# Kernel optimization log

Measured on AMD Instinct MI355X. Metric: run time of the kernel, lower is better.

The kernel has to match this reference:

```python
import jax, jax.numpy as jnp
import numpy as np

N = 50000
E = 500000
H = 128


def _linear(x, w, b):
    # torch nn.Linear: y = x @ W.T + b, W is [out, in]
    return x @ w.T + b


def _layer(x, h, edge_index, w0_w, w0_b, wl_w, wl_b, w1_w, w1_b):
    # PyG MessagePassing(aggr='add', flow='target_to_source'):
    # x_j = h[edge_index[1]], scatter-add into edge_index[0], dim_size = N
    msg = h[edge_index[1]]                               # [E, H] gather
    aggr = jax.ops.segment_sum(msg, edge_index[0], num_segments=h.shape[0])  # [N, H]
    return _linear(aggr, wl_w, wl_b) + _linear(h, w0_w, w0_b) + _linear(x, w1_w, w1_b)


def setup_inputs() -> dict:
    key = jax.random.key(0)
    ks = jax.random.split(key, 12)
    wscale = 0.05
    return {
        "x_a": jax.random.normal(ks[0], (N, H), jnp.float32),
        "x_b": jax.random.normal(ks[1], (N, H), jnp.float32),
        "edge_ab": jax.random.randint(ks[2], (2, E), 0, N, jnp.int32),
        "edge_ba": jax.random.randint(ks[3], (2, E), 0, N, jnp.int32),
        "conv0_w0_w": jax.random.normal(ks[4], (H, H), jnp.float32) * wscale,
        "conv0_w0_b": jnp.zeros((H,), jnp.float32),
        "conv0_wl_w": jax.random.normal(ks[5], (H, H), jnp.float32) * wscale,
        "conv0_wl_b": jnp.zeros((H,), jnp.float32),
        "conv0_w1_w": jax.random.normal(ks[6], (H, H), jnp.float32) * wscale,
        "conv0_w1_b": jnp.zeros((H,), jnp.float32),
        "conv1_w0_w": jax.random.normal(ks[7], (H, H), jnp.float32) * wscale,
        "conv1_w0_b": jnp.zeros((H,), jnp.float32),
        "conv1_wl_w": jax.random.normal(ks[8], (H, H), jnp.float32) * wscale,
        "conv1_wl_b": jnp.zeros((H,), jnp.float32),
        "conv1_w1_w": jax.random.normal(ks[9], (H, H), jnp.float32) * wscale,
        "conv1_w1_b": jnp.zeros((H,), jnp.float32),
        "out_w": jax.random.normal(ks[10], (H, H), jnp.float32) * wscale,
        "out_b": jnp.zeros((H,), jnp.float32),
    }


def reference(x_a, x_b, edge_ab, edge_ba,
              conv0_w0_w, conv0_w0_b, conv0_wl_w, conv0_wl_b, conv0_w1_w, conv0_w1_b,
              conv1_w0_w, conv1_w0_b, conv1_wl_w, conv1_wl_b, conv1_w1_w, conv1_w1_b,
              out_w, out_b):
    # metapath = [(a, r1, b), (b, r2, a)], loop over reversed(metapath):
    # iter 0: conv_idx=1, edge (b, r2, a), dst='a'
    h_a = jax.nn.relu(_layer(x_a, x_a, edge_ba,
                             conv1_w0_w, conv1_w0_b, conv1_wl_w, conv1_wl_b, conv1_w1_w, conv1_w1_b))
    # iter 1: conv_idx=0, edge (a, r1, b), dst='b'
    h_b = jax.nn.relu(_layer(x_b, x_b, edge_ab,
                             conv0_w0_w, conv0_w0_b, conv0_wl_w, conv0_wl_b, conv0_w1_w, conv0_w1_b))
    # start_type = 'a'
    return _linear(h_a, out_w, out_b)
```

## Files before the change

kernel.cpp:

```cpp
#include <hip/hip_runtime.h>
#include <hip/hip_bf16.h>

#define NN 50000
#define NE 500000
#define HD 128
#define CAP 128
#define PREP_B 24
#define ZCUR_B ((NN + 255) / 256)
#define ZAGGR_B 6250
#define K1_B (PREP_B + ZCUR_B + ZAGGR_B)
#define FILLB_B ((NE + 255) / 256)
#define XCONV_B 3125
#define K2_B (FILLB_B + XCONV_B)

typedef __bf16 bf16;
typedef __attribute__((ext_vector_type(8))) __bf16 bf16x8;
typedef __attribute__((ext_vector_type(4))) float floatx4;

__device__ inline float u2f(unsigned int lo16) {
    union { unsigned int i; float f; } c; c.i = lo16 << 16; return c.f;
}

__device__ inline bf16x8 cvt8(floatx4 a, floatx4 b) {
    bf16x8 r;
#pragma unroll
    for (int j = 0; j < 4; j++) { r[j] = (bf16)a[j]; r[j + 4] = (bf16)b[j]; }
    return r;
}

__device__ inline void split8(const floatx4 f0, const floatx4 f1, bf16x8& hi, bf16x8& lo) {
#pragma unroll
    for (int j = 0; j < 4; j++) {
        float a = f0[j]; bf16 h = (bf16)a; hi[j] = h; lo[j] = (bf16)(a - (float)h);
        float b = f1[j]; bf16 g = (bf16)b; hi[j + 4] = g; lo[j + 4] = (bf16)(b - (float)g);
    }
}

__device__ inline bf16x8 zero8() {
    bf16x8 v;
#pragma unroll
    for (int j = 0; j < 8; j++) v[j] = (bf16)0.f;
    return v;
}

__global__ __launch_bounds__(256) void k_setup1(
    const float* __restrict__ wl, const float* __restrict__ w0, const float* __restrict__ w1,
    const float* __restrict__ bl, const float* __restrict__ b0, const float* __restrict__ b1,
    const float* __restrict__ ow, const float* __restrict__ ob,
    bf16* __restrict__ wlb, bf16* __restrict__ w01b, bf16* __restrict__ owb,
    float* __restrict__ bias1, float* __restrict__ bias2,
    float* __restrict__ aggr, int* __restrict__ cur, int tier)
{
    const int b = blockIdx.x, tid = threadIdx.x;
    if (b < PREP_B) {
        int g = b * 256 + tid;
        int m = g >> 11, off = (g & 2047) << 3;
        if (m == 0) {
            const floatx4 a = *(const floatx4*)(wl + off);
            const floatx4 c = *(const floatx4*)(wl + off + 4);
            *(bf16x8*)(wlb + off) = cvt8(a, c);
        } else if (m == 1) {
            floatx4 a = *(const floatx4*)(w0 + off);
            floatx4 c = *(const floatx4*)(w0 + off + 4);
            const floatx4 d = *(const floatx4*)(w1 + off);
            const floatx4 e = *(const floatx4*)(w1 + off + 4);
#pragma unroll
            for (int j = 0; j < 4; j++) { a[j] += d[j]; c[j] += e[j]; }
            *(bf16x8*)(w01b + off) = cvt8(a, c);
        } else {
            const floatx4 a = *(const floatx4*)(ow + off);
            const floatx4 c = *(const floatx4*)(ow + off + 4);
            *(bf16x8*)(owb + off) = cvt8(a, c);
        }
        if (g < 128) bias1[g] = bl[g] + b0[g] + b1[g];
        else if (g < 256) bias2[g - 128] = ob[g - 128];
    } else if (b < PREP_B + ZCUR_B) {
        if (tier >= 1) {
            int i = (b - PREP_B) * 256 + tid;
            if (i < NN) cur[i] = 0;
        }
    } else {
        int i = (b - PREP_B - ZCUR_B) * 256 + tid;
        floatx4 z = {0.f, 0.f, 0.f, 0.f};
        ((floatx4*)aggr)[i] = z;
    }
}

__global__ __launch_bounds__(256) void k_setup2(
    const int* __restrict__ edge, const float* __restrict__ x,
    int* __restrict__ cur, int* __restrict__ bucket, float* __restrict__ aggr,
    bf16* __restrict__ xb)
{
    const int b = blockIdx.x, tid = threadIdx.x;
    if (b < FILLB_B) {
        int e = b * 256 + tid;
        if (e >= NE) return;
        int dst = edge[e];
        int src = edge[NE + e];
        int pos = atomicAdd(&cur[dst], 1);
        if (pos < CAP) {
            bucket[dst * CAP + pos] = src;
        } else {
            const float* xr = x + (size_t)src * HD;
            float* ar = aggr + (size_t)dst * HD;
            for (int c = 0; c < HD; c++) unsafeAtomicAdd(ar + c, xr[c]);
        }
    } else {
        int off = ((b - FILLB_B) * 256 + tid) << 3;
        const floatx4 a = *(const floatx4*)(x + off);
        const floatx4 c = *(const floatx4*)(x + off + 4);
        *(bf16x8*)(xb + off) = cvt8(a, c);
    }
}

__global__ __launch_bounds__(256) void k_aggr(const bf16* __restrict__ xb,
                                              const int* __restrict__ cur,
                                              const int* __restrict__ bucket,
                                              float* __restrict__ aggr) {
    const int gw   = (blockIdx.x * 256 + threadIdx.x) >> 6;
    const int lane = threadIdx.x & 63;
    const int quad = lane >> 4;
    const int ln   = lane & 15;
    const int node = gw * 4 + quad;
    const bool ok  = node < NN;

    float acc[8] = {0.f, 0.f, 0.f, 0.f, 0.f, 0.f, 0.f, 0.f};
    int deg = 0, n = 0;
    const int* bk = bucket;
    if (ok) {
        deg = cur[node];
        n = (deg < CAP) ? deg : CAP;
        bk = bucket + node * CAP;
        if (deg > CAP) {
            const floatx4 s0 = *(const floatx4*)(aggr + node * HD + ln * 8);
            const floatx4 s1 = *(const floatx4*)(aggr + node * HD + ln * 8 + 4);
#pragma unroll
            for (int j = 0; j < 4; j++) { acc[j] = s0[j]; acc[4 + j] = s1[j]; }
        }
    }

    int t = 0;
    for (; t + 3 < n; t += 4) {
        int s0 = bk[t], s1 = bk[t + 1], s2 = bk[t + 2], s3 = bk[t + 3];
        const uint4 v0 = *(const uint4*)(xb + s0 * HD + ln * 8);
        const uint4 v1 = *(const uint4*)(xb + s1 * HD + ln * 8);
        const uint4 v2 = *(const uint4*)(xb + s2 * HD + ln * 8);
        const uint4 v3 = *(const uint4*)(xb + s3 * HD + ln * 8);
        const unsigned int u0[4] = {v0.x, v0.y, v0.z, v0.w};
        const unsigned int u1[4] = {v1.x, v1.y, v1.z, v1.w};
        const unsigned int u2[4] = {v2.x, v2.y, v2.z, v2.w};
        const unsigned int u3[4] = {v3.x, v3.y, v3.z, v3.w};
#pragma unroll
        for (int j = 0; j < 4; j++) {
            acc[2 * j]     += u2f(u0[j] & 0xffff) + u2f(u1[j] & 0xffff)
                            + u2f(u2[j] & 0xffff) + u2f(u3[j] & 0xffff);
            acc[2 * j + 1] += u2f(u0[j] >> 16) + u2f(u1[j] >> 16)
                            + u2f(u2[j] >> 16) + u2f(u3[j] >> 16);
        }
    }
    for (; t < n; t++) {
        const uint4 v = *(const uint4*)(xb + bk[t] * HD + ln * 8);
        const unsigned int u[4] = {v.x, v.y, v.z, v.w};
#pragma unroll
        for (int j = 0; j < 4; j++) {
            acc[2 * j]     += u2f(u[j] & 0xffff);
            acc[2 * j + 1] += u2f(u[j] >> 16);
        }
    }

    if (ok) {
        floatx4 o0, o1;
#pragma unroll
        for (int j = 0; j < 4; j++) { o0[j] = acc[j]; o1[j] = acc[4 + j]; }
        *(floatx4*)(aggr + node * HD + ln * 8) = o0;
        *(floatx4*)(aggr + node * HD + ln * 8 + 4) = o1;
    }
}

__global__ __launch_bounds__(256) void k_scatter(const float* __restrict__ x,
                                                 const int* __restrict__ edge,
                                                 float* __restrict__ aggr) {
    int tid = blockIdx.x * 256 + threadIdx.x;
    int e = tid >> 5;
    int c = (tid & 31) << 2;
    int dst = edge[e];
    int src = edge[NE + e];
    const floatx4 v = *(const floatx4*)(x + src * HD + c);
    float* ap = aggr + dst * HD + c;
    unsafeAtomicAdd(ap + 0, v[0]);
    unsafeAtomicAdd(ap + 1, v[1]);
    unsafeAtomicAdd(ap + 2, v[2]);
    unsafeAtomicAdd(ap + 3, v[3]);
}

__global__ __launch_bounds__(256) void k_gemm12(
    const float* __restrict__ aggr, const float* __restrict__ x, const bf16* __restrict__ xb,
    int use_xb,
    const bf16* __restrict__ wlb, const bf16* __restrict__ w01b, const bf16* __restrict__ owb,
    const float* __restrict__ bias1, const float* __restrict__ bias2,
    float* __restrict__ out)
{
    __shared__ bf16 sA[128 * 136];
    __shared__ bf16 sB[128 * 136];
    __shared__ float b1_s[128], b2_s[128];
    float* tp = (float*)sB;
    const int tid = threadIdx.x;

#pragma unroll
    for (int it = 0; it < 8; it++) {
        int i = tid + it * 256;
        int r = i >> 4;
        int o = (i & 15) << 3;
        *(bf16x8*)(sA + r * 136 + o) = *(const bf16x8*)(wlb  + r * 128 + o);
        *(bf16x8*)(sB + r * 136 + o) = *(const bf16x8*)(w01b + r * 128 + o);
    }
    if (tid < 128) { b1_s[tid] = bias1[tid]; b2_s[tid] = bias2[tid]; }
    __syncthreads();

    const int lane = tid & 63;
    const int wv   = tid >> 6;
    const int ln   = lane & 15;
    const int quad = lane >> 4;
    const int row0 = blockIdx.x * 64 + wv * 16;
    const int arow = row0 + ln;
    const bool aok = arow < NN;

    floatx4 acc[8] = {};

#pragma unroll
    for (int kc = 0; kc < 4; kc++) {
        const int k0 = kc * 32 + quad * 8;
        bf16x8 a_hi = zero8(), a_lo = zero8(), a_x = zero8();
        if (aok) {
            const floatx4 f0 = *(const floatx4*)(aggr + arow * 128 + k0);
            const floatx4 f1 = *(const floatx4*)(aggr + arow * 128 + k0 + 4);
            split8(f0, f1, a_hi, a_lo);
            if (use_xb) {
                a_x = *(const bf16x8*)(xb + arow * 128 + k0);
            } else {
                const floatx4 g0 = *(const floatx4*)(x + arow * 128 + k0);
                const floatx4 g1 = *(const floatx4*)(x + arow * 128 + k0 + 4);
                a_x = cvt8(g0, g1);
            }
        }
#pragma unroll
        for (int nc = 0; nc < 8; nc++) {
            const bf16x8 bw  = *(const bf16x8*)(sA + (nc * 16 + ln) * 136 + k0);
            const bf16x8 bw2 = *(const bf16x8*)(sB + (nc * 16 + ln) * 136 + k0);
            acc[nc] = __builtin_amdgcn_mfma_f32_16x16x32_bf16(a_hi, bw,  acc[nc], 0, 0, 0);
            acc[nc] = __builtin_amdgcn_mfma_f32_16x16x32_bf16(a_lo, bw,  acc[nc], 0, 0, 0);
            acc[nc] = __builtin_amdgcn_mfma_f32_16x16x32_bf16(a_x,  bw2, acc[nc], 0, 0, 0);
        }
    }
    __syncthreads();

#pragma unroll
    for (int it = 0; it < 8; it++) {
        int i = tid + it * 256;
        int r = i >> 4;
        int o = (i & 15) << 3;
        *(bf16x8*)(sA + r * 136 + o) = *(const bf16x8*)(owb + r * 128 + o);
    }
#pragma unroll
    for (int nc = 0; nc < 8; nc++) {
        const int col = nc * 16 + ln;
        const float bv = b1_s[col];
#pragma unroll
        for (int r = 0; r < 4; r++) {
            float v = acc[nc][r] + bv;
            tp[wv * 2112 + (quad * 4 + r) * 132 + col] = (v > 0.f ? v : 0.f);
        }
        acc[nc][0] = acc[nc][1] = acc[nc][2] = acc[nc][3] = 0.f;
    }
    __syncthreads();

#pragma unroll
    for (int kc = 0; kc < 4; kc++) {
        const int k0 = kc * 32 + quad * 8;
        const floatx4 f0 = *(const floatx4*)(tp + wv * 2112 + ln * 132 + k0);
        const floatx4 f1 = *(const floatx4*)(tp + wv * 2112 + ln * 132 + k0 + 4);
        bf16x8 a_hi, a_lo;
        split8(f0, f1, a_hi, a_lo);
#pragma unroll
        for (int nc = 0; nc < 8; nc++) {
            const bf16x8 bw = *(const bf16x8*)(sA + (nc * 16 + ln) * 136 + k0);
            acc[nc] = __builtin_amdgcn_mfma_f32_16x16x32_bf16(a_hi, bw, acc[nc], 0, 0, 0);
            acc[nc] = __builtin_amdgcn_mfma_f32_16x16x32_bf16(a_lo, bw, acc[nc], 0, 0, 0);
        }
    }

#pragma unroll
    for (int nc = 0; nc < 8; nc++) {
        const int col = nc * 16 + ln;
        const float bv = b2_s[col];
#pragma unroll
        for (int r = 0; r < 4; r++) {
            const int row = row0 + quad * 4 + r;
            if (row < NN) out[row * 128 + col] = acc[nc][r] + bv;
        }
    }
}

extern "C" void kernel_launch(void* const* d_in, const int* in_sizes, int n_in,
                              void* d_out, int out_size, void* d_ws, size_t ws_size,
                              hipStream_t stream) {
    const float* x_a     = (const float*)d_in[0];
    const int*   edge_ba = (const int*)d_in[3];
    const float* c1_w0_w = (const float*)d_in[10];
    const float* c1_w0_b = (const float*)d_in[11];
    const float* c1_wl_w = (const float*)d_in[12];
    const float* c1_wl_b = (const float*)d_in[13];
    const float* c1_w1_w = (const float*)d_in[14];
    const float* c1_w1_b = (const float*)d_in[15];
    const float* out_w   = (const float*)d_in[16];
    const float* out_b   = (const float*)d_in[17];

    char* p = (char*)d_ws;
    float* aggr  = (float*)p;   p += (size_t)NN * HD * 4;
    bf16*  wlb   = (bf16*)p;    p += 32768;
    bf16*  w01b  = (bf16*)p;    p += 32768;
    bf16*  owb   = (bf16*)p;    p += 32768;
    float* bias1 = (float*)p;   p += 512;
    float* bias2 = (float*)p;   p += 512;
    const size_t WS_FALL = (size_t)(p - (char*)d_ws);
    int*   cur    = (int*)p;    p += 200704;
    int*   bucket = (int*)p;    p += (size_t)NN * CAP * 4;
    bf16*  xb     = (bf16*)p;   p += (size_t)NN * HD * 2;
    const size_t WS_BUCKET = (size_t)(p - (char*)d_ws);

    const int tier = (ws_size >= WS_BUCKET) ? 1 : 0;

    k_setup1<<<K1_B, 256, 0, stream>>>(c1_wl_w, c1_w0_w, c1_w1_w,
                                       c1_wl_b, c1_w0_b, c1_w1_b,
                                       out_w, out_b,
                                       wlb, w01b, owb, bias1, bias2,
                                       aggr, cur, tier);

    if (tier) {
        k_setup2<<<K2_B, 256, 0, stream>>>(edge_ba, x_a, cur, bucket, aggr, xb);
        k_aggr  <<<3125, 256, 0, stream>>>(xb, cur, bucket, aggr);
    } else {
        k_scatter<<<NE * 32 / 256, 256, 0, stream>>>(x_a, edge_ba, aggr);
    }

    k_gemm12<<<(NN + 63) / 64, 256, 0, stream>>>(aggr, x_a, xb, tier,
                                                 wlb, w01b, owb, bias1, bias2,
                                                 (float*)d_out);
}
```

Baseline: 195.5 us.

## Move x bf16 conversion into setup, shrink bucket cap, prefetch GEMM rows before weights

The x-to-bf16 conversion moves from the bucket-fill kernel into the first setup kernel, so the fill kernel only does edge bucketing. Bucket capacity drops from 128 to 48, which reduces how strided the bucket memory is, at the risk of more overflow edges going through the slow per-channel atomic path. The GEMM kernel now issues its global loads of aggr and x rows before staging weights into shared memory, so the load latency overlaps with the weight staging. The cost is more registers held live across the barrier.

```diff
diff --git a/kernel.cpp b/kernel.cpp
--- a/kernel.cpp
+++ b/kernel.cpp
@@ -4,14 +4,13 @@
 #define NN 50000
 #define NE 500000
 #define HD 128
-#define CAP 128
+#define CAP 48
 #define PREP_B 24
 #define ZCUR_B ((NN + 255) / 256)
 #define ZAGGR_B 6250
-#define K1_B (PREP_B + ZCUR_B + ZAGGR_B)
+#define XCONV_B 3125
+#define K1_B (PREP_B + ZCUR_B + ZAGGR_B + XCONV_B)
 #define FILLB_B ((NE + 255) / 256)
-#define XCONV_B 3125
-#define K2_B (FILLB_B + XCONV_B)
 
 typedef __bf16 bf16;
 typedef __attribute__((ext_vector_type(8))) __bf16 bf16x8;
@@ -47,9 +46,10 @@
     const float* __restrict__ wl, const float* __restrict__ w0, const float* __restrict__ w1,
     const float* __restrict__ bl, const float* __restrict__ b0, const float* __restrict__ b1,
     const float* __restrict__ ow, const float* __restrict__ ob,
+    const float* __restrict__ x,
     bf16* __restrict__ wlb, bf16* __restrict__ w01b, bf16* __restrict__ owb,
     float* __restrict__ bias1, float* __restrict__ bias2,
-    float* __restrict__ aggr, int* __restrict__ cur, int tier)
+    float* __restrict__ aggr, int* __restrict__ cur, bf16* __restrict__ xb, int tier)
 {
     const int b = blockIdx.x, tid = threadIdx.x;
     if (b < PREP_B) {
@@ -79,37 +79,36 @@
             int i = (b - PREP_B) * 256 + tid;
             if (i < NN) cur[i] = 0;
         }
-    } else {
+    } else if (b < PREP_B + ZCUR_B + ZAGGR_B) {
         int i = (b - PREP_B - ZCUR_B) * 256 + tid;
         floatx4 z = {0.f, 0.f, 0.f, 0.f};
         ((floatx4*)aggr)[i] = z;
-    }
-}
-
-__global__ __launch_bounds__(256) void k_setup2(
-    const int* __restrict__ edge, const float* __restrict__ x,
-    int* __restrict__ cur, int* __restrict__ bucket, float* __restrict__ aggr,
-    bf16* __restrict__ xb)
-{
-    const int b = blockIdx.x, tid = threadIdx.x;
-    if (b < FILLB_B) {
-        int e = b * 256 + tid;
-        if (e >= NE) return;
-        int dst = edge[e];
-        int src = edge[NE + e];
-        int pos = atomicAdd(&cur[dst], 1);
-        if (pos < CAP) {
-            bucket[dst * CAP + pos] = src;
-        } else {
-            const float* xr = x + (size_t)src * HD;
-            float* ar = aggr + (size_t)dst * HD;
-            for (int c = 0; c < HD; c++) unsafeAtomicAdd(ar + c, xr[c]);
-        }
     } else {
-        int off = ((b - FILLB_B) * 256 + tid) << 3;
-        const floatx4 a = *(const floatx4*)(x + off);
-        const floatx4 c = *(const floatx4*)(x + off + 4);
-        *(bf16x8*)(xb + off) = cvt8(a, c);
+        if (tier >= 1) {
+            int off = ((b - PREP_B - ZCUR_B - ZAGGR_B) * 256 + tid) << 3;
+            const floatx4 a = *(const floatx4*)(x + off);
+            const floatx4 c = *(const floatx4*)(x + off + 4);
+            *(bf16x8*)(xb + off) = cvt8(a, c);
+        }
+    }
+}
+
+__global__ __launch_bounds__(256) void k_fillb(const int* __restrict__ edge,
+                                               const float* __restrict__ x,
+                                               int* __restrict__ cur,
+                                               int* __restrict__ bucket,
+                                               float* __restrict__ aggr) {
+    int e = blockIdx.x * 256 + threadIdx.x;
+    if (e >= NE) return;
+    int dst = edge[e];
+    int src = edge[NE + e];
+    int pos = atomicAdd(&cur[dst], 1);
+    if (pos < CAP) {
+        bucket[dst * CAP + pos] = src;
+    } else {
+        const float* xr = x + (size_t)src * HD;
+        float* ar = aggr + (size_t)dst * HD;
+        for (int c = 0; c < HD; c++) unsafeAtomicAdd(ar + c, xr[c]);
     }
 }
 
@@ -206,17 +205,6 @@
     float* tp = (float*)sB;
     const int tid = threadIdx.x;
 
-#pragma unroll
-    for (int it = 0; it < 8; it++) {
-        int i = tid + it * 256;
-        int r = i >> 4;
-        int o = (i & 15) << 3;
-        *(bf16x8*)(sA + r * 136 + o) = *(const bf16x8*)(wlb  + r * 128 + o);
-        *(bf16x8*)(sB + r * 136 + o) = *(const bf16x8*)(w01b + r * 128 + o);
-    }
-    if (tid < 128) { b1_s[tid] = bias1[tid]; b2_s[tid] = bias2[tid]; }
-    __syncthreads();
-
     const int lane = tid & 63;
     const int wv   = tid >> 6;
     const int ln   = lane & 15;
@@ -225,31 +213,55 @@
     const int arow = row0 + ln;
     const bool aok = arow < NN;
 
-    floatx4 acc[8] = {};
-
-#pragma unroll
-    for (int kc = 0; kc < 4; kc++) {
-        const int k0 = kc * 32 + quad * 8;
-        bf16x8 a_hi = zero8(), a_lo = zero8(), a_x = zero8();
-        if (aok) {
-            const floatx4 f0 = *(const floatx4*)(aggr + arow * 128 + k0);
-            const floatx4 f1 = *(const floatx4*)(aggr + arow * 128 + k0 + 4);
-            split8(f0, f1, a_hi, a_lo);
+    floatx4 fa[8];
+    bf16x8  ax[4];
+    if (aok) {
+#pragma unroll
+        for (int kc = 0; kc < 4; kc++) {
+            const int k0 = kc * 32 + quad * 8;
+            fa[2 * kc]     = *(const floatx4*)(aggr + arow * 128 + k0);
+            fa[2 * kc + 1] = *(const floatx4*)(aggr + arow * 128 + k0 + 4);
             if (use_xb) {
-                a_x = *(const bf16x8*)(xb + arow * 128 + k0);
+                ax[kc] = *(const bf16x8*)(xb + arow * 128 + k0);
             } else {
                 const floatx4 g0 = *(const floatx4*)(x + arow * 128 + k0);
                 const floatx4 g1 = *(const floatx4*)(x + arow * 128 + k0 + 4);
-                a_x = cvt8(g0, g1);
+                ax[kc] = cvt8(g0, g1);
             }
         }
+    } else {
+#pragma unroll
+        for (int kc = 0; kc < 4; kc++) {
+            floatx4 z = {0.f, 0.f, 0.f, 0.f};
+            fa[2 * kc] = z; fa[2 * kc + 1] = z; ax[kc] = zero8();
+        }
+    }
+
+#pragma unroll
+    for (int it = 0; it < 8; it++) {
+        int i = tid + it * 256;
+        int r = i >> 4;
+        int o = (i & 15) << 3;
+        *(bf16x8*)(sA + r * 136 + o) = *(const bf16x8*)(wlb  + r * 128 + o);
+        *(bf16x8*)(sB + r * 136 + o) = *(const bf16x8*)(w01b + r * 128 + o);
+    }
+    if (tid < 128) { b1_s[tid] = bias1[tid]; b2_s[tid] = bias2[tid]; }
+    __syncthreads();
+
+    floatx4 acc[8] = {};
+
+#pragma unroll
+    for (int kc = 0; kc < 4; kc++) {
+        const int k0 = kc * 32 + quad * 8;
+        bf16x8 a_hi, a_lo;
+        split8(fa[2 * kc], fa[2 * kc + 1], a_hi, a_lo);
 #pragma unroll
         for (int nc = 0; nc < 8; nc++) {
             const bf16x8 bw  = *(const bf16x8*)(sA + (nc * 16 + ln) * 136 + k0);
             const bf16x8 bw2 = *(const bf16x8*)(sB + (nc * 16 + ln) * 136 + k0);
-            acc[nc] = __builtin_amdgcn_mfma_f32_16x16x32_bf16(a_hi, bw,  acc[nc], 0, 0, 0);
-            acc[nc] = __builtin_amdgcn_mfma_f32_16x16x32_bf16(a_lo, bw,  acc[nc], 0, 0, 0);
-            acc[nc] = __builtin_amdgcn_mfma_f32_16x16x32_bf16(a_x,  bw2, acc[nc], 0, 0, 0);
+            acc[nc] = __builtin_amdgcn_mfma_f32_16x16x32_bf16(a_hi,  bw,  acc[nc], 0, 0, 0);
+            acc[nc] = __builtin_amdgcn_mfma_f32_16x16x32_bf16(a_lo,  bw,  acc[nc], 0, 0, 0);
+            acc[nc] = __builtin_amdgcn_mfma_f32_16x16x32_bf16(ax[kc], bw2, acc[nc], 0, 0, 0);
         }
     }
     __syncthreads();
@@ -332,13 +344,13 @@
 
     k_setup1<<<K1_B, 256, 0, stream>>>(c1_wl_w, c1_w0_w, c1_w1_w,
                                        c1_wl_b, c1_w0_b, c1_w1_b,
-                                       out_w, out_b,
+                                       out_w, out_b, x_a,
                                        wlb, w01b, owb, bias1, bias2,
-                                       aggr, cur, tier);
+                                       aggr, cur, xb, tier);
 
     if (tier) {
-        k_setup2<<<K2_B, 256, 0, stream>>>(edge_ba, x_a, cur, bucket, aggr, xb);
-        k_aggr  <<<3125, 256, 0, stream>>>(xb, cur, bucket, aggr);
+        k_fillb<<<FILLB_B, 256, 0, stream>>>(edge_ba, x_a, cur, bucket, aggr);
+        k_aggr <<<3125, 256, 0, stream>>>(xb, cur, bucket, aggr);
     } else {
         k_scatter<<<NE * 32 / 256, 256, 0, stream>>>(x_a, edge_ba, aggr);
     }
```

After: 197.8 us. About the same (+1.2%).
